# Performance work log

Hardware: AMD Instinct MI355X
Metric: run time of the kernel (lower is better)

Reference implementation:

```python
import jax, jax.numpy as jnp
import numpy as np

N = 100000   # nodes
E = 640000   # edges
F = 128      # num_features
D = 128      # dim
G = 128      # graphs in batch
BN_EPS = 1e-5


def setup_inputs() -> dict:
    key = jax.random.key(0)
    ks = jax.random.split(key, 16)
    lin = lambda k, i, o: (jax.random.normal(k, (i, o), jnp.float32) / np.sqrt(i)).astype(jnp.float32)
    inp = {
        "x": jax.random.normal(ks[0], (N, F), jnp.float32),
        "edge_index": jax.random.randint(ks[1], (2, E), 0, N),
        "batch": jnp.sort(jax.random.randint(ks[2], (N,), 0, G)),
        # layer 0: Linear(F,D)-ReLU-Linear(D,D), BN(D)
        "W0a": lin(ks[3], F, D), "b0a": jnp.zeros((D,), jnp.float32),
        "W0b": lin(ks[4], D, D), "b0b": jnp.zeros((D,), jnp.float32),
        "g0": jnp.ones((D,), jnp.float32), "be0": jnp.zeros((D,), jnp.float32),
        # layer 1: Linear(D,D)-ReLU-Linear(D,D), BN(D)
        "W1a": lin(ks[5], D, D), "b1a": jnp.zeros((D,), jnp.float32),
        "W1b": lin(ks[6], D, D), "b1b": jnp.zeros((D,), jnp.float32),
        "g1": jnp.ones((D,), jnp.float32), "be1": jnp.zeros((D,), jnp.float32),
        # layer 2: Linear(D,D)-ReLU-Linear(D,1), BN(1)
        "W2a": lin(ks[7], D, D), "b2a": jnp.zeros((D,), jnp.float32),
        "W2b": lin(ks[8], D, 1), "b2b": jnp.zeros((1,), jnp.float32),
        "g2": jnp.ones((1,), jnp.float32), "be2": jnp.zeros((1,), jnp.float32),
    }
    return inp


def _gin_layer(x, src, dst, Wa, ba, Wb, bb, g, be, relu_out):
    # GINConv (eps=0): h = x + sum_{j in N(i)} x_j, then MLP, then BN (train-mode stats)
    agg = jax.ops.segment_sum(x[src], dst, num_segments=N)
    h = x + agg
    h = jax.nn.relu(h @ Wa + ba) @ Wb + bb
    mu = jnp.mean(h, axis=0)
    var = jnp.mean((h - mu) ** 2, axis=0)  # biased var (torch BN normalization)
    h = (h - mu) * jax.lax.rsqrt(var + BN_EPS) * g + be
    return jax.nn.relu(h) if relu_out else h


def reference(x, edge_index, batch,
              W0a, b0a, W0b, b0b, g0, be0,
              W1a, b1a, W1b, b1b, g1, be1,
              W2a, b2a, W2b, b2b, g2, be2):
    src, dst = edge_index[0], edge_index[1]
    h = _gin_layer(x, src, dst, W0a, b0a, W0b, b0b, g0, be0, True)
    h = _gin_layer(h, src, dst, W1a, b1a, W1b, b1b, g1, be1, True)
    h = _gin_layer(h, src, dst, W2a, b2a, W2b, b2b, g2, be2, False)  # [N,1], no final ReLU
    # segment softmax over graphs, temperature 5.0 (PyG softmax semantics)
    z = h / 5.0
    m = jax.ops.segment_max(z, batch, num_segments=G)
    ez = jnp.exp(z - m[batch])
    s = jax.ops.segment_sum(ez, batch, num_segments=G)
    return ez / (s[batch] + 1e-16)
```

## Files before the change

kernel.cpp:

```cpp
#include <hip/hip_runtime.h>
#include <math.h>

#define NN 100000
#define EE 640000
#define GG 128
#define BN_EPS 1e-5f
#define NBLK 98

typedef __attribute__((ext_vector_type(8))) short short8;
typedef __attribute__((ext_vector_type(4))) float f32x4;


__device__ __forceinline__ short f2bf(float f) {
    unsigned u = __float_as_uint(f);
    u += 0x7fffu + ((u >> 16) & 1);
    return (short)(u >> 16);
}
__device__ __forceinline__ float bf2f(short s) {
    return __uint_as_float(((unsigned)(unsigned short)s) << 16);
}
__device__ __forceinline__ int swz(int row, int chunk) {
    return row * 128 + ((chunk ^ (row & 15)) << 3);
}
__device__ __forceinline__ int swze(int row, int col) {
    return row * 128 + (((col >> 3) ^ (row & 15)) << 3) + (col & 7);
}

__global__ void k_setup(const float* __restrict__ x,
                        const float* __restrict__ W0a, const float* __restrict__ W0b,
                        const float* __restrict__ W1a, const float* __restrict__ W1b,
                        const float* __restrict__ W2a, short* __restrict__ Wt,
                        short* __restrict__ Xbf, int* __restrict__ deg,
                        float* __restrict__ smf) {
    int idx = blockIdx.x * 256 + threadIdx.x;
    if (idx < 81920) {
        int wi = idx >> 14, r = idx & 16383;
        const float* W = (wi == 0) ? W0a : (wi == 1) ? W0b : (wi == 2) ? W1a
                        : (wi == 3) ? W1b : W2a;
        int k = r >> 7, n = r & 127;
        Wt[wi * 16384 + n * 128 + k] = f2bf(W[k * 128 + n]);
    }
    if (idx < NN) deg[idx] = 0;
    if (idx < 4112) smf[idx] = 0.0f;
    if (idx < 1600000) {
        const float4* xr = (const float4*)x + (size_t)idx * 2;
        float4 v0 = xr[0], v1 = xr[1];
        short8 o;
        o[0] = f2bf(v0.x); o[1] = f2bf(v0.y); o[2] = f2bf(v0.z); o[3] = f2bf(v0.w);
        o[4] = f2bf(v1.x); o[5] = f2bf(v1.y); o[6] = f2bf(v1.z); o[7] = f2bf(v1.w);
        *(short8*)(Xbf + (size_t)idx * 8) = o;
    }
}

__global__ void k_hist(const int* __restrict__ ei, int* __restrict__ deg) {
    int e = blockIdx.x * 256 + threadIdx.x;
    if (e < EE) atomicAdd(&deg[ei[EE + e]], 1);
}

__global__ __launch_bounds__(1024) void k_scan1(const int* __restrict__ deg,
                                                int* __restrict__ offs,
                                                int* __restrict__ bsums) {
    __shared__ int sm[1024];
    int t = threadIdx.x;
    int i = blockIdx.x * 1024 + t;
    int v = (i < NN) ? deg[i] : 0;
    sm[t] = v;
    __syncthreads();
    for (int off = 1; off < 1024; off <<= 1) {
        int add = (t >= off) ? sm[t - off] : 0;
        __syncthreads();
        sm[t] += add;
        __syncthreads();
    }
    if (i < NN) offs[i] = sm[t] - v;
    if (t == 1023) bsums[blockIdx.x] = sm[1023];
}

__global__ void k_scan2(int* bsums) {
    __shared__ int sm[128];
    int t = threadIdx.x;
    int v = (t < NBLK) ? bsums[t] : 0;
    sm[t] = v;
    __syncthreads();
    for (int off = 1; off < 128; off <<= 1) {
        int add = (t >= off) ? sm[t - off] : 0;
        __syncthreads();
        sm[t] += add;
        __syncthreads();
    }
    if (t < NBLK) bsums[t] = sm[t] - v;
}

__global__ __launch_bounds__(1024) void k_scan3(int* __restrict__ offs,
                                                const int* __restrict__ bsums,
                                                int* __restrict__ pos) {
    int t = threadIdx.x;
    int i = blockIdx.x * 1024 + t;
    if (i < NN) {
        int o = offs[i] + bsums[blockIdx.x];
        offs[i] = o;
        pos[i] = o;
    }
    if (i == 0) offs[NN] = EE;
}

__global__ void k_fill(const int* __restrict__ ei, int* __restrict__ pos,
                       int* __restrict__ csr) {
    int e = blockIdx.x * 256 + threadIdx.x;
    if (e < EE) {
        int d = ei[EE + e];
        int p = atomicAdd(&pos[d], 1);
        csr[p] = ei[e];
    }
}

template <bool BN>
__global__ void k_gather(const short* __restrict__ h, const int* __restrict__ offs,
                         const int* __restrict__ csr, const float* __restrict__ rep,
                         const float* __restrict__ g, const float* __restrict__ be,
                         short* __restrict__ agg) {
    __shared__ float parS[128], parH[128];
    int t = threadIdx.x;
    if constexpr (BN) {
        if (t < 128) {
            float s = 0.f, ss = 0.f;
#pragma unroll
            for (int r = 0; r < 8; ++r) {
                s += rep[r * 256 + t];
                ss += rep[r * 256 + 128 + t];
            }
            const float inv = 1.0f / (float)NN;
            float mu = s * inv;
            float var = ss * inv - mu * mu;
            float sc = g[t] / sqrtf(var + BN_EPS);
            parS[t] = sc;
            parH[t] = be[t] - mu * sc;
        }
        __syncthreads();
    }
    int tt = blockIdx.x * 256 + t;
    int n = tt >> 4, l = t & 15;
    if (n >= NN) return;
    float sc[8], sh[8];
    if constexpr (BN) {
#pragma unroll
        for (int j = 0; j < 8; ++j) { sc[j] = parS[l * 8 + j]; sh[j] = parH[l * 8 + j]; }
    }
    int j0 = offs[n], j1 = offs[n + 1];
    short8 v = *(const short8*)(h + (size_t)n * 128 + l * 8);
    float f[8];
#pragma unroll
    for (int j = 0; j < 8; ++j)
        f[j] = BN ? fmaxf(fmaf(bf2f(v[j]), sc[j], sh[j]), 0.f) : bf2f(v[j]);
    int j = j0;
    for (; j + 3 < j1; j += 4) {
        int s0 = csr[j], s1 = csr[j + 1], s2 = csr[j + 2], s3 = csr[j + 3];
        short8 w0 = *(const short8*)(h + (size_t)s0 * 128 + l * 8);
        short8 w1 = *(const short8*)(h + (size_t)s1 * 128 + l * 8);
        short8 w2 = *(const short8*)(h + (size_t)s2 * 128 + l * 8);
        short8 w3 = *(const short8*)(h + (size_t)s3 * 128 + l * 8);
#pragma unroll
        for (int k = 0; k < 8; ++k) {
            if constexpr (BN) {
                f[k] += fmaxf(fmaf(bf2f(w0[k]), sc[k], sh[k]), 0.f)
                      + fmaxf(fmaf(bf2f(w1[k]), sc[k], sh[k]), 0.f)
                      + fmaxf(fmaf(bf2f(w2[k]), sc[k], sh[k]), 0.f)
                      + fmaxf(fmaf(bf2f(w3[k]), sc[k], sh[k]), 0.f);
            } else {
                f[k] += bf2f(w0[k]) + bf2f(w1[k]) + bf2f(w2[k]) + bf2f(w3[k]);
            }
        }
    }
    for (; j < j1; ++j) {
        int s0 = csr[j];
        short8 w0 = *(const short8*)(h + (size_t)s0 * 128 + l * 8);
#pragma unroll
        for (int k = 0; k < 8; ++k)
            f[k] += BN ? fmaxf(fmaf(bf2f(w0[k]), sc[k], sh[k]), 0.f) : bf2f(w0[k]);
    }
    short8 o;
#pragma unroll
    for (int k = 0; k < 8; ++k) o[k] = f2bf(f[k]);
    *(short8*)(agg + (size_t)n * 128 + l * 8) = o;
}

template <bool SECOND>
__global__ __launch_bounds__(256, 3) void k_mlp(const short* __restrict__ hin,
                                                const short* __restrict__ Wta,
                                                const float* __restrict__ ba,
                                                const short* __restrict__ Wtb,
                                                const float* __restrict__ bb,
                                                short* __restrict__ hout,
                                                float* __restrict__ statsRep,
                                                const float* __restrict__ w2,
                                                const float* __restrict__ b2,
                                                float* __restrict__ z,
                                                float* __restrict__ s2rep) {
    __shared__ short Asb[8192];
    __shared__ short Wsb[16384];
    __shared__ float redS[512];
    const int t = threadIdx.x;
    const int row0 = blockIdx.x * 64;
    const int lane = t & 63, wave = t >> 6;
    const int r16 = lane & 15, q = lane >> 4;
    const int rh = wave & 1, ch = wave >> 1;
    const int RA = rh * 32, CB = ch * 64;

    short8 wpre[8];
#pragma unroll
    for (int i = 0; i < 8; ++i) {
        int f = i * 256 + t;
        int r = f >> 4, c8 = f & 15;
        if (i < 4) {
            int gr = row0 + r;
            short8 v = {0, 0, 0, 0, 0, 0, 0, 0};
            if (gr < NN) v = *(const short8*)(hin + (size_t)gr * 128 + c8 * 8);
            *(short8*)&Asb[swz(r, c8)] = v;
        }
        *(short8*)&Wsb[swz(r, c8)] = *(const short8*)(Wta + r * 128 + c8 * 8);
        if constexpr (SECOND) wpre[i] = *(const short8*)(Wtb + r * 128 + c8 * 8);
    }
    __syncthreads();

    f32x4 acc[2][4];
#pragma unroll
    for (int rt = 0; rt < 2; ++rt)
#pragma unroll
        for (int ct = 0; ct < 4; ++ct) acc[rt][ct] = (f32x4)0.f;

#pragma unroll
    for (int kk = 0; kk < 4; ++kk) {
        short8 b[4], a[2];
#pragma unroll
        for (int ct = 0; ct < 4; ++ct)
            b[ct] = *(const short8*)&Wsb[swz(CB + ct * 16 + r16, kk * 4 + q)];
#pragma unroll
        for (int rt = 0; rt < 2; ++rt)
            a[rt] = *(const short8*)&Asb[swz(RA + rt * 16 + r16, kk * 4 + q)];
#pragma unroll
        for (int rt = 0; rt < 2; ++rt)
#pragma unroll
            for (int ct = 0; ct < 4; ++ct)
                acc[rt][ct] = __builtin_amdgcn_mfma_f32_16x16x32_bf16(a[rt], b[ct], acc[rt][ct], 0, 0, 0);
    }
    __syncthreads();

    float bav[4];
#pragma unroll
    for (int ct = 0; ct < 4; ++ct) bav[ct] = ba[CB + ct * 16 + r16];
#pragma unroll
    for (int rt = 0; rt < 2; ++rt)
#pragma unroll
        for (int ct = 0; ct < 4; ++ct)
#pragma unroll
            for (int rg = 0; rg < 4; ++rg) {
                float m = fmaxf(acc[rt][ct][rg] + bav[ct], 0.f);
                Asb[swze(RA + rt * 16 + q * 4 + rg, CB + ct * 16 + r16)] = f2bf(m);
            }

    if constexpr (!SECOND) {
        __syncthreads();
        const int l16 = t & 15, rr = t >> 4;
        float4 w0 = ((const float4*)w2)[l16 * 2];
        float4 w1 = ((const float4*)w2)[l16 * 2 + 1];
        float b2v = b2[0];
        float s = 0.f, ss = 0.f;
#pragma unroll
        for (int pass = 0; pass < 4; ++pass) {
            int r = pass * 16 + rr;
            int gr = row0 + r;
            short8 v = *(const short8*)&Asb[swz(r, l16)];
            float p = bf2f(v[0]) * w0.x + bf2f(v[1]) * w0.y + bf2f(v[2]) * w0.z +
                      bf2f(v[3]) * w0.w + bf2f(v[4]) * w1.x + bf2f(v[5]) * w1.y +
                      bf2f(v[6]) * w1.z + bf2f(v[7]) * w1.w;
#pragma unroll
            for (int off = 1; off < 16; off <<= 1) p += __shfl_xor(p, off, 16);
            if (l16 == 0 && gr < NN) {
                float h2 = p + b2v;
                z[gr] = h2;
                s += h2;
                ss += h2 * h2;
            }
        }
        s += __shfl_xor(s, 16); s += __shfl_xor(s, 32);
        ss += __shfl_xor(ss, 16); ss += __shfl_xor(ss, 32);
        if ((t & 63) == 0) { redS[wave * 2] = s; redS[wave * 2 + 1] = ss; }
        __syncthreads();
        if (t == 0) {
            float S = redS[0] + redS[2] + redS[4] + redS[6];
            float SS = redS[1] + redS[3] + redS[5] + redS[7];
            int rp = (blockIdx.x & 7) * 2;
            unsafeAtomicAdd(&s2rep[rp], S);
            unsafeAtomicAdd(&s2rep[rp + 1], SS);
        }
        return;
    } else {
#pragma unroll
        for (int i = 0; i < 8; ++i) {
            int f = i * 256 + t;
            int r = f >> 4, c8 = f & 15;
            *(short8*)&Wsb[swz(r, c8)] = wpre[i];
        }
        __syncthreads();

#pragma unroll
        for (int rt = 0; rt < 2; ++rt)
#pragma unroll
            for (int ct = 0; ct < 4; ++ct) acc[rt][ct] = (f32x4)0.f;

#pragma unroll
        for (int kk = 0; kk < 4; ++kk) {
            short8 b[4], a[2];
#pragma unroll
            for (int ct = 0; ct < 4; ++ct)
                b[ct] = *(const short8*)&Wsb[swz(CB + ct * 16 + r16, kk * 4 + q)];
#pragma unroll
            for (int rt = 0; rt < 2; ++rt)
                a[rt] = *(const short8*)&Asb[swz(RA + rt * 16 + r16, kk * 4 + q)];
#pragma unroll
            for (int rt = 0; rt < 2; ++rt)
#pragma unroll
                for (int ct = 0; ct < 4; ++ct)
                    acc[rt][ct] = __builtin_amdgcn_mfma_f32_16x16x32_bf16(a[rt], b[ct], acc[rt][ct], 0, 0, 0);
        }
        __syncthreads();

        float bbv[4];
#pragma unroll
        for (int ct = 0; ct < 4; ++ct) bbv[ct] = bb[CB + ct * 16 + r16];
        float s[4] = {0.f, 0.f, 0.f, 0.f}, ss[4] = {0.f, 0.f, 0.f, 0.f};
#pragma unroll
        for (int rt = 0; rt < 2; ++rt)
#pragma unroll
            for (int ct = 0; ct < 4; ++ct)
#pragma unroll
                for (int rg = 0; rg < 4; ++rg) {
                    int lr = RA + rt * 16 + q * 4 + rg;
                    int gr = row0 + lr;
                    float hv = acc[rt][ct][rg] + bbv[ct];
                    if (gr < NN) { s[ct] += hv; ss[ct] += hv * hv; }
                    Asb[swze(lr, CB + ct * 16 + r16)] = f2bf(hv);
                }
#pragma unroll
        for (int ct = 0; ct < 4; ++ct) {
            s[ct] += __shfl_xor(s[ct], 16);
            s[ct] += __shfl_xor(s[ct], 32);
            ss[ct] += __shfl_xor(ss[ct], 16);
            ss[ct] += __shfl_xor(ss[ct], 32);
        }
        if (lane < 16) {
#pragma unroll
            for (int ct = 0; ct < 4; ++ct) {
                int col = CB + ct * 16 + r16;
                redS[rh * 256 + col] = s[ct];
                redS[rh * 256 + 128 + col] = ss[ct];
            }
        }
        __syncthreads();
        {
            float v = redS[t] + redS[256 + t];
            unsafeAtomicAdd(&statsRep[(blockIdx.x & 7) * 256 + t], v);
        }
#pragma unroll
        for (int i = 0; i < 4; ++i) {
            int f = i * 256 + t;
            int r = f >> 4, c8 = f & 15;
            int gr = row0 + r;
            if (gr < NN)
                *(short8*)(hout + (size_t)gr * 128 + c8 * 8) = *(const short8*)&Asb[swz(r, c8)];
        }
    }
}

__device__ __forceinline__ int lbound(const int* __restrict__ b, int val) {
    int lo = 0, hi = NN;
    while (lo < hi) {
        int m = (lo + hi) >> 1;
        if (b[m] < val) lo = m + 1; else hi = m;
    }
    return lo;
}

__global__ void k_softmax(const float* __restrict__ zr, const float* __restrict__ s2rep,
                          const float* __restrict__ g2, const float* __restrict__ be2,
                          const int* __restrict__ batch, float* __restrict__ out) {
    __shared__ float rb[4];
    const int g = blockIdx.x, t = threadIdx.x;
    const int lo = lbound(batch, g), hi = lbound(batch, g + 1);
    float s = 0.f, ssq = 0.f;
#pragma unroll
    for (int i = 0; i < 8; ++i) { s += s2rep[i * 2]; ssq += s2rep[i * 2 + 1]; }
    const float mu = s / (float)NN;
    const float var = ssq / (float)NN - mu * mu;
    const float sc = g2[0] / sqrtf(var + BN_EPS) * 0.2f;
    const float sh = (be2[0] - mu * g2[0] / sqrtf(var + BN_EPS)) * 0.2f;

    float m = -INFINITY;
    for (int i = lo + t; i < hi; i += 256) m = fmaxf(m, fmaf(zr[i], sc, sh));
#pragma unroll
    for (int off = 1; off < 64; off <<= 1) m = fmaxf(m, __shfl_xor(m, off, 64));
    if ((t & 63) == 0) rb[t >> 6] = m;
    __syncthreads();
    float gmax = fmaxf(fmaxf(rb[0], rb[1]), fmaxf(rb[2], rb[3]));
    __syncthreads();

    float sum = 0.f;
    for (int i = lo + t; i < hi; i += 256) {
        float e = expf(fmaf(zr[i], sc, sh) - gmax);
        out[i] = e;
        sum += e;
    }
#pragma unroll
    for (int off = 1; off < 64; off <<= 1) sum += __shfl_xor(sum, off, 64);
    if ((t & 63) == 0) rb[t >> 6] = sum;
    __syncthreads();
    float S = rb[0] + rb[1] + rb[2] + rb[3];
    float inv = 1.0f / (S + 1e-16f);
    for (int i = lo + t; i < hi; i += 256) out[i] *= inv;
}

extern "C" void kernel_launch(void* const* d_in, const int* in_sizes, int n_in,
                              void* d_out, int out_size, void* d_ws, size_t ws_size,
                              hipStream_t stream) {
    const float* x   = (const float*)d_in[0];
    const int* ei    = (const int*)d_in[1];
    const int* batch = (const int*)d_in[2];
    const float *W0a = (const float*)d_in[3],  *b0a = (const float*)d_in[4];
    const float *W0b = (const float*)d_in[5],  *b0b = (const float*)d_in[6];
    const float *g0  = (const float*)d_in[7],  *be0 = (const float*)d_in[8];
    const float *W1a = (const float*)d_in[9],  *b1a = (const float*)d_in[10];
    const float *W1b = (const float*)d_in[11], *b1b = (const float*)d_in[12];
    const float *g1  = (const float*)d_in[13], *be1 = (const float*)d_in[14];
    const float *W2a = (const float*)d_in[15], *b2a = (const float*)d_in[16];
    const float *W2b = (const float*)d_in[17], *b2b = (const float*)d_in[18];
    const float *g2  = (const float*)d_in[19], *be2 = (const float*)d_in[20];
    float* out = (float*)d_out;

    char* wsb = (char*)d_ws;
    short* Abf = (short*)wsb;
    short* Bbf = (short*)(wsb + 25600000);
    float* Zb  = (float*)(wsb + 51200000);
    float* SMf = (float*)(wsb + 51600000);
    float* S0r = SMf;
    float* S1r = SMf + 2048;
    float* S2r = SMf + 4096;
    int* offs  = (int*)(wsb + 51620000);
    int* bsums = (int*)(wsb + 52020004);
    int* csr   = (int*)(wsb + 52020516);
    short* Wt  = (short*)(wsb + 54580544);
    short* Xbf = (short*)(wsb + 54744384);
    int* deg = (int*)wsb;
    int* pos = (int*)(wsb + 400000);

    const int gE   = (EE + 255) / 256;
    const int gG16 = (NN * 16) / 256;
    const int gMlp = (NN + 63) / 64;

    k_setup<<<6250, 256, 0, stream>>>(x, W0a, W0b, W1a, W1b, W2a, Wt, Xbf, deg, SMf);

    k_hist<<<gE, 256, 0, stream>>>(ei, deg);
    k_scan1<<<NBLK, 1024, 0, stream>>>(deg, offs, bsums);
    k_scan2<<<1, 128, 0, stream>>>(bsums);
    k_scan3<<<NBLK, 1024, 0, stream>>>(offs, bsums, pos);
    k_fill<<<gE, 256, 0, stream>>>(ei, pos, csr);

    k_gather<false><<<gG16, 256, 0, stream>>>(Xbf, offs, csr, nullptr, nullptr, nullptr, Abf);
    k_mlp<true><<<gMlp, 256, 0, stream>>>(Abf, Wt, b0a, Wt + 16384, b0b, Abf, S0r,
                                          nullptr, nullptr, nullptr, nullptr);
    k_gather<true><<<gG16, 256, 0, stream>>>(Abf, offs, csr, S0r, g0, be0, Bbf);
    k_mlp<true><<<gMlp, 256, 0, stream>>>(Bbf, Wt + 2 * 16384, b1a, Wt + 3 * 16384, b1b,
                                          Bbf, S1r, nullptr, nullptr, nullptr, nullptr);
    k_gather<true><<<gG16, 256, 0, stream>>>(Bbf, offs, csr, S1r, g1, be1, Abf);
    k_mlp<false><<<gMlp, 256, 0, stream>>>(Abf, Wt + 4 * 16384, b2a, nullptr, nullptr,
                                           nullptr, nullptr, W2b, b2b, Zb, S2r);

    k_softmax<<<GG, 256, 0, stream>>>(Zb, S2r, g2, be2, batch, out);
}
```

Before: 401.2 us.

## Fuse neighbor gather into MLP kernel and fold scan2 into scan3

Merges the per-layer CSR gather-sum (with BN+ReLU of the previous layer) directly into the MLP kernel, so the aggregated features go straight into shared memory instead of making a round trip through global memory. Blocks grow to 512 threads covering 128 rows each. The separate bsums scan kernel is removed; each scan3 block now computes its own prefix serially. This cuts launches and global traffic, but the gather and the MFMA work now share occupancy and LDS (64KB+ per block), which could reduce latency hiding for the irregular gather.

```diff
diff --git a/kernel.cpp b/kernel.cpp
--- a/kernel.cpp
+++ b/kernel.cpp
@@ -76,28 +76,23 @@
     if (t == 1023) bsums[blockIdx.x] = sm[1023];
 }
 
-__global__ void k_scan2(int* bsums) {
-    __shared__ int sm[128];
-    int t = threadIdx.x;
-    int v = (t < NBLK) ? bsums[t] : 0;
-    sm[t] = v;
-    __syncthreads();
-    for (int off = 1; off < 128; off <<= 1) {
-        int add = (t >= off) ? sm[t - off] : 0;
-        __syncthreads();
-        sm[t] += add;
-        __syncthreads();
-    }
-    if (t < NBLK) bsums[t] = sm[t] - v;
-}
-
 __global__ __launch_bounds__(1024) void k_scan3(int* __restrict__ offs,
                                                 const int* __restrict__ bsums,
                                                 int* __restrict__ pos) {
+    __shared__ int smb[128];
+    __shared__ int baseS;
     int t = threadIdx.x;
+    if (t < 128) smb[t] = (t < NBLK) ? bsums[t] : 0;
+    __syncthreads();
+    if (t == 0) {
+        int b = 0;
+        for (int i = 0; i < (int)blockIdx.x; ++i) b += smb[i];
+        baseS = b;
+    }
+    __syncthreads();
     int i = blockIdx.x * 1024 + t;
     if (i < NN) {
-        int o = offs[i] + bsums[blockIdx.x];
+        int o = offs[i] + baseS;
         offs[i] = o;
         pos[i] = o;
     }
@@ -114,14 +109,36 @@
     }
 }
 
-template <bool BN>
-__global__ void k_gather(const short* __restrict__ h, const int* __restrict__ offs,
-                         const int* __restrict__ csr, const float* __restrict__ rep,
-                         const float* __restrict__ g, const float* __restrict__ be,
-                         short* __restrict__ agg) {
+template <int MODE>
+__global__ __launch_bounds__(512, 4) void k_gmlp(const short* __restrict__ hin,
+                                                 const int* __restrict__ offs,
+                                                 const int* __restrict__ csr,
+                                                 const float* __restrict__ rep,
+                                                 const float* __restrict__ g,
+                                                 const float* __restrict__ be,
+                                                 const short* __restrict__ Wta,
+                                                 const float* __restrict__ ba,
+                                                 const short* __restrict__ Wtb,
+                                                 const float* __restrict__ bb,
+                                                 short* __restrict__ hout,
+                                                 float* __restrict__ statsRep,
+                                                 const float* __restrict__ w2,
+                                                 const float* __restrict__ b2,
+                                                 float* __restrict__ z,
+                                                 float* __restrict__ s2rep) {
+    __shared__ short Asb[16384];
+    __shared__ short Wsb[16384];
     __shared__ float parS[128], parH[128];
-    int t = threadIdx.x;
-    if constexpr (BN) {
+    __shared__ float redS[1024];
+    const int t = threadIdx.x;
+    const int row0 = blockIdx.x * 128;
+    const int lane = t & 63, wave = t >> 6;
+    const int r16 = lane & 15, q = lane >> 4;
+    const int rh = wave & 3, ch = wave >> 2;
+    const int RA = rh * 32, CB = ch * 64;
+    const int l = t & 15;
+
+    if constexpr (MODE != 0) {
         if (t < 128) {
             float s = 0.f, ss = 0.f;
 #pragma unroll
@@ -138,87 +155,64 @@
         }
         __syncthreads();
     }
-    int tt = blockIdx.x * 256 + t;
-    int n = tt >> 4, l = t & 15;
-    if (n >= NN) return;
-    float sc[8], sh[8];
-    if constexpr (BN) {
-#pragma unroll
-        for (int j = 0; j < 8; ++j) { sc[j] = parS[l * 8 + j]; sh[j] = parH[l * 8 + j]; }
-    }
-    int j0 = offs[n], j1 = offs[n + 1];
-    short8 v = *(const short8*)(h + (size_t)n * 128 + l * 8);
-    float f[8];
-#pragma unroll
-    for (int j = 0; j < 8; ++j)
-        f[j] = BN ? fmaxf(fmaf(bf2f(v[j]), sc[j], sh[j]), 0.f) : bf2f(v[j]);
-    int j = j0;
-    for (; j + 3 < j1; j += 4) {
-        int s0 = csr[j], s1 = csr[j + 1], s2 = csr[j + 2], s3 = csr[j + 3];
-        short8 w0 = *(const short8*)(h + (size_t)s0 * 128 + l * 8);
-        short8 w1 = *(const short8*)(h + (size_t)s1 * 128 + l * 8);
-        short8 w2 = *(const short8*)(h + (size_t)s2 * 128 + l * 8);
-        short8 w3 = *(const short8*)(h + (size_t)s3 * 128 + l * 8);
-#pragma unroll
-        for (int k = 0; k < 8; ++k) {
-            if constexpr (BN) {
-                f[k] += fmaxf(fmaf(bf2f(w0[k]), sc[k], sh[k]), 0.f)
-                      + fmaxf(fmaf(bf2f(w1[k]), sc[k], sh[k]), 0.f)
-                      + fmaxf(fmaf(bf2f(w2[k]), sc[k], sh[k]), 0.f)
-                      + fmaxf(fmaf(bf2f(w3[k]), sc[k], sh[k]), 0.f);
-            } else {
-                f[k] += bf2f(w0[k]) + bf2f(w1[k]) + bf2f(w2[k]) + bf2f(w3[k]);
-            }
-        }
-    }
-    for (; j < j1; ++j) {
-        int s0 = csr[j];
-        short8 w0 = *(const short8*)(h + (size_t)s0 * 128 + l * 8);
-#pragma unroll
-        for (int k = 0; k < 8; ++k)
-            f[k] += BN ? fmaxf(fmaf(bf2f(w0[k]), sc[k], sh[k]), 0.f) : bf2f(w0[k]);
-    }
-    short8 o;
-#pragma unroll
-    for (int k = 0; k < 8; ++k) o[k] = f2bf(f[k]);
-    *(short8*)(agg + (size_t)n * 128 + l * 8) = o;
-}
-
-template <bool SECOND>
-__global__ __launch_bounds__(256, 3) void k_mlp(const short* __restrict__ hin,
-                                                const short* __restrict__ Wta,
-                                                const float* __restrict__ ba,
-                                                const short* __restrict__ Wtb,
-                                                const float* __restrict__ bb,
-                                                short* __restrict__ hout,
-                                                float* __restrict__ statsRep,
-                                                const float* __restrict__ w2,
-                                                const float* __restrict__ b2,
-                                                float* __restrict__ z,
-                                                float* __restrict__ s2rep) {
-    __shared__ short Asb[8192];
-    __shared__ short Wsb[16384];
-    __shared__ float redS[512];
-    const int t = threadIdx.x;
-    const int row0 = blockIdx.x * 64;
-    const int lane = t & 63, wave = t >> 6;
-    const int r16 = lane & 15, q = lane >> 4;
-    const int rh = wave & 1, ch = wave >> 1;
-    const int RA = rh * 32, CB = ch * 64;
-
-    short8 wpre[8];
-#pragma unroll
-    for (int i = 0; i < 8; ++i) {
-        int f = i * 256 + t;
+
+    short8 wpre[4];
+#pragma unroll
+    for (int i = 0; i < 4; ++i) {
+        int f = i * 512 + t;
         int r = f >> 4, c8 = f & 15;
-        if (i < 4) {
-            int gr = row0 + r;
-            short8 v = {0, 0, 0, 0, 0, 0, 0, 0};
-            if (gr < NN) v = *(const short8*)(hin + (size_t)gr * 128 + c8 * 8);
-            *(short8*)&Asb[swz(r, c8)] = v;
-        }
         *(short8*)&Wsb[swz(r, c8)] = *(const short8*)(Wta + r * 128 + c8 * 8);
-        if constexpr (SECOND) wpre[i] = *(const short8*)(Wtb + r * 128 + c8 * 8);
+        if constexpr (MODE != 2) wpre[i] = *(const short8*)(Wtb + r * 128 + c8 * 8);
+    }
+
+    float sc8[8], sh8[8];
+    if constexpr (MODE != 0) {
+#pragma unroll
+        for (int j = 0; j < 8; ++j) { sc8[j] = parS[l * 8 + j]; sh8[j] = parH[l * 8 + j]; }
+    }
+#pragma unroll
+    for (int p = 0; p < 4; ++p) {
+        int r = p * 32 + (t >> 4);
+        int gr = row0 + r;
+        float f8[8] = {0.f, 0.f, 0.f, 0.f, 0.f, 0.f, 0.f, 0.f};
+        if (gr < NN) {
+            int j0 = offs[gr], j1 = offs[gr + 1];
+            short8 v = *(const short8*)(hin + (size_t)gr * 128 + l * 8);
+#pragma unroll
+            for (int k = 0; k < 8; ++k)
+                f8[k] = (MODE != 0) ? fmaxf(fmaf(bf2f(v[k]), sc8[k], sh8[k]), 0.f) : bf2f(v[k]);
+            int j = j0;
+            for (; j + 3 < j1; j += 4) {
+                int s0 = csr[j], s1 = csr[j + 1], s2 = csr[j + 2], s3 = csr[j + 3];
+                short8 w0 = *(const short8*)(hin + (size_t)s0 * 128 + l * 8);
+                short8 w1 = *(const short8*)(hin + (size_t)s1 * 128 + l * 8);
+                short8 w2v = *(const short8*)(hin + (size_t)s2 * 128 + l * 8);
+                short8 w3 = *(const short8*)(hin + (size_t)s3 * 128 + l * 8);
+#pragma unroll
+                for (int k = 0; k < 8; ++k) {
+                    if constexpr (MODE != 0) {
+                        f8[k] += fmaxf(fmaf(bf2f(w0[k]), sc8[k], sh8[k]), 0.f)
+                               + fmaxf(fmaf(bf2f(w1[k]), sc8[k], sh8[k]), 0.f)
+                               + fmaxf(fmaf(bf2f(w2v[k]), sc8[k], sh8[k]), 0.f)
+                               + fmaxf(fmaf(bf2f(w3[k]), sc8[k], sh8[k]), 0.f);
+                    } else {
+                        f8[k] += bf2f(w0[k]) + bf2f(w1[k]) + bf2f(w2v[k]) + bf2f(w3[k]);
+                    }
+                }
+            }
+            for (; j < j1; ++j) {
+                int s0 = csr[j];
+                short8 w0 = *(const short8*)(hin + (size_t)s0 * 128 + l * 8);
+#pragma unroll
+                for (int k = 0; k < 8; ++k)
+                    f8[k] += (MODE != 0) ? fmaxf(fmaf(bf2f(w0[k]), sc8[k], sh8[k]), 0.f)
+                                         : bf2f(w0[k]);
+            }
+        }
+        short8 o;
+#pragma unroll
+        for (int k = 0; k < 8; ++k) o[k] = f2bf(f8[k]);
+        *(short8*)&Asb[swz(r, l)] = o;
     }
     __syncthreads();
 
@@ -227,7 +221,6 @@
     for (int rt = 0; rt < 2; ++rt)
 #pragma unroll
         for (int ct = 0; ct < 4; ++ct) acc[rt][ct] = (f32x4)0.f;
-
 #pragma unroll
     for (int kk = 0; kk < 4; ++kk) {
         short8 b[4], a[2];
@@ -257,26 +250,34 @@
                 float m = fmaxf(acc[rt][ct][rg] + bav[ct], 0.f);
                 Asb[swze(RA + rt * 16 + q * 4 + rg, CB + ct * 16 + r16)] = f2bf(m);
             }
-
-    if constexpr (!SECOND) {
-        __syncthreads();
-        const int l16 = t & 15, rr = t >> 4;
-        float4 w0 = ((const float4*)w2)[l16 * 2];
-        float4 w1 = ((const float4*)w2)[l16 * 2 + 1];
+    if constexpr (MODE != 2) {
+#pragma unroll
+        for (int i = 0; i < 4; ++i) {
+            int f = i * 512 + t;
+            int r = f >> 4, c8 = f & 15;
+            *(short8*)&Wsb[swz(r, c8)] = wpre[i];
+        }
+    }
+    __syncthreads();
+
+    if constexpr (MODE == 2) {
+        const int rr = t >> 4;
+        float4 w0 = ((const float4*)w2)[l * 2];
+        float4 w1 = ((const float4*)w2)[l * 2 + 1];
         float b2v = b2[0];
         float s = 0.f, ss = 0.f;
 #pragma unroll
-        for (int pass = 0; pass < 4; ++pass) {
-            int r = pass * 16 + rr;
+        for (int p = 0; p < 4; ++p) {
+            int r = p * 32 + rr;
             int gr = row0 + r;
-            short8 v = *(const short8*)&Asb[swz(r, l16)];
-            float p = bf2f(v[0]) * w0.x + bf2f(v[1]) * w0.y + bf2f(v[2]) * w0.z +
-                      bf2f(v[3]) * w0.w + bf2f(v[4]) * w1.x + bf2f(v[5]) * w1.y +
-                      bf2f(v[6]) * w1.z + bf2f(v[7]) * w1.w;
-#pragma unroll
-            for (int off = 1; off < 16; off <<= 1) p += __shfl_xor(p, off, 16);
-            if (l16 == 0 && gr < NN) {
-                float h2 = p + b2v;
+            short8 v = *(const short8*)&Asb[swz(r, l)];
+            float pp = bf2f(v[0]) * w0.x + bf2f(v[1]) * w0.y + bf2f(v[2]) * w0.z +
+                       bf2f(v[3]) * w0.w + bf2f(v[4]) * w1.x + bf2f(v[5]) * w1.y +
+                       bf2f(v[6]) * w1.z + bf2f(v[7]) * w1.w;
+#pragma unroll
+            for (int off = 1; off < 16; off <<= 1) pp += __shfl_xor(pp, off, 16);
+            if (l == 0 && gr < NN) {
+                float h2 = pp + b2v;
                 z[gr] = h2;
                 s += h2;
                 ss += h2 * h2;
@@ -287,8 +288,9 @@
         if ((t & 63) == 0) { redS[wave * 2] = s; redS[wave * 2 + 1] = ss; }
         __syncthreads();
         if (t == 0) {
-            float S = redS[0] + redS[2] + redS[4] + redS[6];
-            float SS = redS[1] + redS[3] + redS[5] + redS[7];
+            float S = 0.f, SS = 0.f;
+#pragma unroll
+            for (int w = 0; w < 8; ++w) { S += redS[w * 2]; SS += redS[w * 2 + 1]; }
             int rp = (blockIdx.x & 7) * 2;
             unsafeAtomicAdd(&s2rep[rp], S);
             unsafeAtomicAdd(&s2rep[rp + 1], SS);
@@ -296,18 +298,9 @@
         return;
     } else {
 #pragma unroll
-        for (int i = 0; i < 8; ++i) {
-            int f = i * 256 + t;
-            int r = f >> 4, c8 = f & 15;
-            *(short8*)&Wsb[swz(r, c8)] = wpre[i];
-        }
-        __syncthreads();
-
-#pragma unroll
         for (int rt = 0; rt < 2; ++rt)
 #pragma unroll
             for (int ct = 0; ct < 4; ++ct) acc[rt][ct] = (f32x4)0.f;
-
 #pragma unroll
         for (int kk = 0; kk < 4; ++kk) {
             short8 b[4], a[2];
@@ -357,13 +350,13 @@
             }
         }
         __syncthreads();
-        {
-            float v = redS[t] + redS[256 + t];
+        if (t < 256) {
+            float v = redS[t] + redS[256 + t] + redS[512 + t] + redS[768 + t];
             unsafeAtomicAdd(&statsRep[(blockIdx.x & 7) * 256 + t], v);
         }
 #pragma unroll
         for (int i = 0; i < 4; ++i) {
-            int f = i * 256 + t;
+            int f = i * 512 + t;
             int r = f >> 4, c8 = f & 15;
             int gr = row0 + r;
             if (gr < NN)
@@ -452,27 +445,25 @@
     int* deg = (int*)wsb;
     int* pos = (int*)(wsb + 400000);
 
-    const int gE   = (EE + 255) / 256;
-    const int gG16 = (NN * 16) / 256;
-    const int gMlp = (NN + 63) / 64;
+    const int gE    = (EE + 255) / 256;
+    const int gGmlp = (NN + 127) / 128;
 
     k_setup<<<6250, 256, 0, stream>>>(x, W0a, W0b, W1a, W1b, W2a, Wt, Xbf, deg, SMf);
 
     k_hist<<<gE, 256, 0, stream>>>(ei, deg);
     k_scan1<<<NBLK, 1024, 0, stream>>>(deg, offs, bsums);
-    k_scan2<<<1, 128, 0, stream>>>(bsums);
     k_scan3<<<NBLK, 1024, 0, stream>>>(offs, bsums, pos);
     k_fill<<<gE, 256, 0, stream>>>(ei, pos, csr);
 
-    k_gather<false><<<gG16, 256, 0, stream>>>(Xbf, offs, csr, nullptr, nullptr, nullptr, Abf);
-    k_mlp<true><<<gMlp, 256, 0, stream>>>(Abf, Wt, b0a, Wt + 16384, b0b, Abf, S0r,
-                                          nullptr, nullptr, nullptr, nullptr);
-    k_gather<true><<<gG16, 256, 0, stream>>>(Abf, offs, csr, S0r, g0, be0, Bbf);
-    k_mlp<true><<<gMlp, 256, 0, stream>>>(Bbf, Wt + 2 * 16384, b1a, Wt + 3 * 16384, b1b,
-                                          Bbf, S1r, nullptr, nullptr, nullptr, nullptr);
-    k_gather<true><<<gG16, 256, 0, stream>>>(Bbf, offs, csr, S1r, g1, be1, Abf);
-    k_mlp<false><<<gMlp, 256, 0, stream>>>(Abf, Wt + 4 * 16384, b2a, nullptr, nullptr,
-                                           nullptr, nullptr, W2b, b2b, Zb, S2r);
+    k_gmlp<0><<<gGmlp, 512, 0, stream>>>(Xbf, offs, csr, nullptr, nullptr, nullptr,
+                                         Wt, b0a, Wt + 16384, b0b, Abf, S0r,
+                                         nullptr, nullptr, nullptr, nullptr);
+    k_gmlp<1><<<gGmlp, 512, 0, stream>>>(Abf, offs, csr, S0r, g0, be0,
+                                         Wt + 2 * 16384, b1a, Wt + 3 * 16384, b1b, Bbf, S1r,
+                                         nullptr, nullptr, nullptr, nullptr);
+    k_gmlp<2><<<gGmlp, 512, 0, stream>>>(Bbf, offs, csr, S1r, g1, be1,
+                                         Wt + 4 * 16384, b2a, nullptr, nullptr,
+                                         nullptr, nullptr, W2b, b2b, Zb, S2r);
 
     k_softmax<<<GG, 256, 0, stream>>>(Zb, S2r, g2, be2, batch, out);
 }
```

Result: faster. 373.2 us, median of 2 (-7.0%).
